# Kernel optimization log

Hardware: AMD Instinct MI355X
Metric: run time of the kernel (lower is better)

The kernel has to match this reference:

```python
import jax, jax.numpy as jnp
import numpy as np

N_NODES = 100000
N_EDGES = 1600000
C_IN, C_HID, C_OUT = 64, 64, 32


def _gcn_conv(x, src, dst, ew, W, b, n_nodes):
    """PyG GCNConv: add self-loops (weight 1), symmetric normalization,
    out[dst] += norm * (x @ W)[src], plus bias. Dropout omitted (eval mode)."""
    h = x @ W  # [N, C_out_layer]
    loop = jnp.arange(n_nodes, dtype=src.dtype)
    src_a = jnp.concatenate([src, loop])
    dst_a = jnp.concatenate([dst, loop])
    ew_a = jnp.concatenate([ew, jnp.ones((n_nodes,), dtype=ew.dtype)])
    # degree over incoming (dst) side, weighted
    deg = jax.ops.segment_sum(ew_a, dst_a, num_segments=n_nodes)
    dinv = jnp.where(deg > 0, jax.lax.rsqrt(deg), 0.0)
    norm = dinv[src_a] * ew_a * dinv[dst_a]  # [E+N]
    msg = h[src_a] * norm[:, None]           # gather + scale: [E+N, C]
    out = jax.ops.segment_sum(msg, dst_a, num_segments=n_nodes)  # scatter-add
    return out + b


def setup_inputs() -> dict:
    key = jax.random.key(0)
    k1, k2, k3, k4, k5, k6, k7 = jax.random.split(key, 7)
    x = jax.random.normal(k1, (N_NODES, C_IN), dtype=jnp.float32)
    edge_index = jax.random.randint(k2, (2, N_EDGES), 0, N_NODES, dtype=jnp.int64)
    edge_attr = jax.random.uniform(k3, (N_EDGES,), dtype=jnp.float32)
    s1 = 1.0 / np.sqrt(C_IN)
    s2 = 1.0 / np.sqrt(C_HID)
    W1 = jax.random.uniform(k4, (C_IN, C_HID), jnp.float32, -s1, s1)
    b1 = jnp.zeros((C_HID,), dtype=jnp.float32)
    W2 = jax.random.uniform(k5, (C_HID, C_OUT), jnp.float32, -s2, s2)
    b2 = jnp.zeros((C_OUT,), dtype=jnp.float32)
    return {"x": x, "edge_index": edge_index, "edge_attr": edge_attr,
            "W1": W1, "b1": b1, "W2": W2, "b2": b2}


def reference(x, edge_index, edge_attr, W1, b1, W2, b2):
    n = x.shape[0]
    src, dst = edge_index[0], edge_index[1]
    h = _gcn_conv(x, src, dst, edge_attr, W1, b1, n)
    h = jax.nn.relu(h)  # dropout is identity in eval mode
    out = _gcn_conv(h, src, dst, edge_attr, W2, b2, n)
    return out
```

## Files before the change

kernel.cpp:

```cpp
#include <hip/hip_runtime.h>
#include <hip/hip_fp16.h>


#define TPB 256
#define TPB_P 512
#define TPB_S 1024
#define BSH2 9
#define BN2 512
#define NBC 256
#define PCHUNK 4096
#define CAP2 9728

typedef union { uint2 u; __half2 h[2]; } hpack;
typedef union { uint4 u; __half2 h[4]; } hpack8;
typedef union { int4 q; int2 p[2]; } epack;

__global__ __launch_bounds__(256) void k_binit(int* __restrict__ bpos) {
  int i = threadIdx.x;
  if (i < NBC) bpos[i] = i * CAP2;
}

__global__ __launch_bounds__(TPB_P) void k_part(const int* __restrict__ si,
                                                const int* __restrict__ di,
                                                const float* __restrict__ ew,
                                                int* __restrict__ bpos,
                                                int2* __restrict__ tin, int e) {
  __shared__ int hcnt[NBC];
  __shared__ int lst0[NBC];
  __shared__ int lcur[NBC];
  __shared__ int hbase[NBC];
  __shared__ int2 se[PCHUNK];
  __shared__ unsigned char sbk[PCHUNK];
  int t = threadIdx.x;
  int lo = blockIdx.x * PCHUNK;
  int hi = lo + PCHUNK; if (hi > e) hi = e;
  int cn = hi - lo;
  if (t < NBC) hcnt[t] = 0;
  __syncthreads();
  for (int i = lo + t; i < hi; i += TPB_P) atomicAdd(&hcnt[di[i] >> BSH2], 1);
  __syncthreads();
  int c = (t < NBC) ? hcnt[t] : 0;
  for (int off = 1; off < NBC; off <<= 1) {
    int u = (t >= off && t < NBC) ? hcnt[t - off] : 0;
    __syncthreads();
    if (t < NBC) hcnt[t] += u;
    __syncthreads();
  }
  if (t < NBC) {
    int ex = hcnt[t] - c;
    lst0[t] = ex;
    lcur[t] = 0;
    hbase[t] = c ? atomicAdd(&bpos[t], c) : 0;
  }
  __syncthreads();
  for (int i = lo + t; i < hi; i += TPB_P) {
    int d = di[i];
    int bk = d >> BSH2;
    int loc = atomicAdd(&lcur[bk], 1);
    int p = lst0[bk] + loc;
    se[p] = make_int2(si[i] | ((d & (BN2 - 1)) << 17), __float_as_int(ew[i]));
    sbk[p] = (unsigned char)bk;
  }
  __syncthreads();
  for (int p = t; p < cn; p += TPB_P) {
    int bk = sbk[p];
    tin[hbase[bk] + (p - lst0[bk])] = se[p];
  }
}

__global__ __launch_bounds__(TPB_S) void k_sortb(const int2* __restrict__ tin,
                                                 const int* __restrict__ bpos,
                                                 int2* __restrict__ colpk,
                                                 int2* __restrict__ rowseg,
                                                 float* __restrict__ dinv, int n) {
  __shared__ int cnt[BN2];
  __shared__ float degw[BN2];
  __shared__ int cur[BN2];
  __shared__ int ls[BN2];
  int b = blockIdx.x, t = threadIdx.x;
  if (t < BN2) { cnt[t] = 0; degw[t] = 1.0f; }
  __syncthreads();
  int jb = b * CAP2, je = bpos[b];
  for (int j = jb + t; j < je; j += TPB_S) {
    int2 p = tin[j];
    int dl = p.x >> 17;
    atomicAdd(&cnt[dl], 1);
    atomicAdd(&degw[dl], __int_as_float(p.y));
  }
  __syncthreads();
  int c = (t < BN2) ? cnt[t] : 0;
  int c2 = (c + 1) & ~1;
  if (t < BN2) ls[t] = c2;
  __syncthreads();
  for (int off = 1; off < BN2; off <<= 1) {
    int u = (t >= off && t < BN2) ? ls[t - off] : 0;
    __syncthreads();
    if (t < BN2) ls[t] += u;
    __syncthreads();
  }
  int base = b << BSH2;
  if (t < BN2) {
    int start = jb + ls[t] - c2;
    cur[t] = start;
    int node = base + t;
    if (node < n) {
      rowseg[node] = make_int2(start, start + c2);
      dinv[node] = rsqrtf(degw[t]);
    }
    if (c & 1) colpk[start + c] = make_int2(0, 0);
  }
  __syncthreads();
  for (int j = jb + t; j < je; j += TPB_S) {
    int2 p = tin[j];
    int dl = p.x >> 17;
    int pos = atomicAdd(&cur[dl], 1);
    colpk[pos] = make_int2(p.x & 0x1FFFF, p.y);
  }
}

__global__ __launch_bounds__(TPB) void k_gemm1(const float* __restrict__ x,
                                               const float* __restrict__ W1,
                                               const float* __restrict__ dinv,
                                               __half* __restrict__ g1h, int n) {
  __shared__ float Wl[64 * 64];
  int t = threadIdx.x;
  {
    const float4* W4 = (const float4*)W1;
    float4* Wl4 = (float4*)Wl;
#pragma unroll
    for (int i = 0; i < 4; ++i) Wl4[t + TPB * i] = W4[t + TPB * i];
  }
  __syncthreads();
  int r = blockIdx.x * 16 + (t >> 4);
  if (r >= n) return;
  int c0 = (t & 15) << 2;
  const float4* xr = (const float4*)(x + (size_t)r * 64);
  float ax = 0.f, ay = 0.f, az = 0.f, aw = 0.f;
#pragma unroll
  for (int kk = 0; kk < 16; ++kk) {
    float4 xv = xr[kk];
    const float* w = &Wl[(kk * 4) * 64 + c0];
    float4 w0 = *(const float4*)(w);
    float4 w1 = *(const float4*)(w + 64);
    float4 w2 = *(const float4*)(w + 128);
    float4 w3 = *(const float4*)(w + 192);
    ax += xv.x * w0.x + xv.y * w1.x + xv.z * w2.x + xv.w * w3.x;
    ay += xv.x * w0.y + xv.y * w1.y + xv.z * w2.y + xv.w * w3.y;
    az += xv.x * w0.z + xv.y * w1.z + xv.z * w2.z + xv.w * w3.z;
    aw += xv.x * w0.w + xv.y * w1.w + xv.z * w2.w + xv.w * w3.w;
  }
  float dv = dinv[r];
  hpack pk;
  pk.h[0] = __floats2half2_rn(dv * ax, dv * ay);
  pk.h[1] = __floats2half2_rn(dv * az, dv * aw);
  *(uint2*)(g1h + (size_t)r * 64 + c0) = pk.u;
}

__global__ __launch_bounds__(TPB) void k_gather64(const __half* __restrict__ g1h,
                                                  const int2* __restrict__ colpk,
                                                  const int2* __restrict__ rowseg,
                                                  float* __restrict__ acc, int n) {
  int t = threadIdx.x;
  int r = blockIdx.x * 32 + (t >> 3);
  if (r >= n) return;
  int c0 = (t & 7) << 3;
  float a[8];
  {
    hpack8 s; s.u = *(const uint4*)(g1h + (size_t)r * 64 + c0);
#pragma unroll
    for (int k = 0; k < 4; ++k) {
      float2 f = __half22float2(s.h[k]);
      a[2 * k] = f.x; a[2 * k + 1] = f.y;
    }
  }
  int2 seg = rowseg[r];
  int j = seg.x;
  for (; j + 7 < seg.y; j += 8) {
    epack q0; q0.q = *(const int4*)(colpk + j);
    epack q1; q1.q = *(const int4*)(colpk + j + 2);
    epack q2; q2.q = *(const int4*)(colpk + j + 4);
    epack q3; q3.q = *(const int4*)(colpk + j + 6);
    hpack8 u0; u0.u = *(const uint4*)(g1h + (size_t)q0.p[0].x * 64 + c0);
    hpack8 u1; u1.u = *(const uint4*)(g1h + (size_t)q0.p[1].x * 64 + c0);
    hpack8 u2; u2.u = *(const uint4*)(g1h + (size_t)q1.p[0].x * 64 + c0);
    hpack8 u3; u3.u = *(const uint4*)(g1h + (size_t)q1.p[1].x * 64 + c0);
    hpack8 u4; u4.u = *(const uint4*)(g1h + (size_t)q2.p[0].x * 64 + c0);
    hpack8 u5; u5.u = *(const uint4*)(g1h + (size_t)q2.p[1].x * 64 + c0);
    hpack8 u6; u6.u = *(const uint4*)(g1h + (size_t)q3.p[0].x * 64 + c0);
    hpack8 u7; u7.u = *(const uint4*)(g1h + (size_t)q3.p[1].x * 64 + c0);
    float w0 = __int_as_float(q0.p[0].y), w1 = __int_as_float(q0.p[1].y);
    float w2 = __int_as_float(q1.p[0].y), w3 = __int_as_float(q1.p[1].y);
    float w4 = __int_as_float(q2.p[0].y), w5 = __int_as_float(q2.p[1].y);
    float w6 = __int_as_float(q3.p[0].y), w7 = __int_as_float(q3.p[1].y);
#pragma unroll
    for (int k = 0; k < 4; ++k) {
      float2 f;
      f = __half22float2(u0.h[k]); a[2*k] += w0 * f.x; a[2*k+1] += w0 * f.y;
      f = __half22float2(u1.h[k]); a[2*k] += w1 * f.x; a[2*k+1] += w1 * f.y;
      f = __half22float2(u2.h[k]); a[2*k] += w2 * f.x; a[2*k+1] += w2 * f.y;
      f = __half22float2(u3.h[k]); a[2*k] += w3 * f.x; a[2*k+1] += w3 * f.y;
      f = __half22float2(u4.h[k]); a[2*k] += w4 * f.x; a[2*k+1] += w4 * f.y;
      f = __half22float2(u5.h[k]); a[2*k] += w5 * f.x; a[2*k+1] += w5 * f.y;
      f = __half22float2(u6.h[k]); a[2*k] += w6 * f.x; a[2*k+1] += w6 * f.y;
      f = __half22float2(u7.h[k]); a[2*k] += w7 * f.x; a[2*k+1] += w7 * f.y;
    }
  }
  for (; j + 1 < seg.y; j += 2) {
    epack q0; q0.q = *(const int4*)(colpk + j);
    float w0 = __int_as_float(q0.p[0].y), w1 = __int_as_float(q0.p[1].y);
    hpack8 u0; u0.u = *(const uint4*)(g1h + (size_t)q0.p[0].x * 64 + c0);
    hpack8 u1; u1.u = *(const uint4*)(g1h + (size_t)q0.p[1].x * 64 + c0);
#pragma unroll
    for (int k = 0; k < 4; ++k) {
      float2 f;
      f = __half22float2(u0.h[k]); a[2*k] += w0 * f.x; a[2*k+1] += w0 * f.y;
      f = __half22float2(u1.h[k]); a[2*k] += w1 * f.x; a[2*k+1] += w1 * f.y;
    }
  }
  float* op = acc + (size_t)r * 64 + c0;
  *(float4*)(op)     = make_float4(a[0], a[1], a[2], a[3]);
  *(float4*)(op + 4) = make_float4(a[4], a[5], a[6], a[7]);
}

__global__ __launch_bounds__(TPB) void k_gemm2(const float* __restrict__ acc1,
                                               const float* __restrict__ W2,
                                               const float* __restrict__ b1,
                                               const float* __restrict__ dinv,
                                               __half* __restrict__ g2h, int n) {
  __shared__ float Wl[64 * 32];
  __shared__ float b1l[64];
  int t = threadIdx.x;
  {
    const float4* W4 = (const float4*)W2;
    float4* Wl4 = (float4*)Wl;
#pragma unroll
    for (int i = 0; i < 2; ++i) Wl4[t + TPB * i] = W4[t + TPB * i];
    if (t < 64) b1l[t] = b1[t];
  }
  __syncthreads();
  int r = blockIdx.x * 32 + (t >> 3);
  if (r >= n) return;
  int c0 = (t & 7) << 2;
  float dv = dinv[r];
  const float4* ar = (const float4*)(acc1 + (size_t)r * 64);
  float ax = 0.f, ay = 0.f, az = 0.f, aw = 0.f;
#pragma unroll
  for (int kk = 0; kk < 16; ++kk) {
    float4 v = ar[kk];
    float x0 = fmaxf(dv * v.x + b1l[4 * kk + 0], 0.f);
    float x1 = fmaxf(dv * v.y + b1l[4 * kk + 1], 0.f);
    float x2 = fmaxf(dv * v.z + b1l[4 * kk + 2], 0.f);
    float x3 = fmaxf(dv * v.w + b1l[4 * kk + 3], 0.f);
    const float* w = &Wl[(kk * 4) * 32 + c0];
    float4 w0 = *(const float4*)(w);
    float4 w1 = *(const float4*)(w + 32);
    float4 w2 = *(const float4*)(w + 64);
    float4 w3 = *(const float4*)(w + 96);
    ax += x0 * w0.x + x1 * w1.x + x2 * w2.x + x3 * w3.x;
    ay += x0 * w0.y + x1 * w1.y + x2 * w2.y + x3 * w3.y;
    az += x0 * w0.z + x1 * w1.z + x2 * w2.z + x3 * w3.z;
    aw += x0 * w0.w + x1 * w1.w + x2 * w2.w + x3 * w3.w;
  }
  hpack pk;
  pk.h[0] = __floats2half2_rn(dv * ax, dv * ay);
  pk.h[1] = __floats2half2_rn(dv * az, dv * aw);
  *(uint2*)(g2h + (size_t)r * 32 + c0) = pk.u;
}

__global__ __launch_bounds__(TPB) void k_gather32(const __half* __restrict__ g2h,
                                                  const int2* __restrict__ colpk,
                                                  const int2* __restrict__ rowseg,
                                                  const float* __restrict__ dinv,
                                                  const float* __restrict__ b2,
                                                  float* __restrict__ out, int n) {
  int t = threadIdx.x;
  int r = blockIdx.x * 64 + (t >> 2);
  if (r >= n) return;
  int c0 = (t & 3) << 3;
  float a[8];
  {
    hpack8 s; s.u = *(const uint4*)(g2h + (size_t)r * 32 + c0);
#pragma unroll
    for (int k = 0; k < 4; ++k) {
      float2 f = __half22float2(s.h[k]);
      a[2 * k] = f.x; a[2 * k + 1] = f.y;
    }
  }
  int2 seg = rowseg[r];
  int j = seg.x;
  for (; j + 7 < seg.y; j += 8) {
    epack q0; q0.q = *(const int4*)(colpk + j);
    epack q1; q1.q = *(const int4*)(colpk + j + 2);
    epack q2; q2.q = *(const int4*)(colpk + j + 4);
    epack q3; q3.q = *(const int4*)(colpk + j + 6);
    hpack8 u0; u0.u = *(const uint4*)(g2h + (size_t)q0.p[0].x * 32 + c0);
    hpack8 u1; u1.u = *(const uint4*)(g2h + (size_t)q0.p[1].x * 32 + c0);
    hpack8 u2; u2.u = *(const uint4*)(g2h + (size_t)q1.p[0].x * 32 + c0);
    hpack8 u3; u3.u = *(const uint4*)(g2h + (size_t)q1.p[1].x * 32 + c0);
    hpack8 u4; u4.u = *(const uint4*)(g2h + (size_t)q2.p[0].x * 32 + c0);
    hpack8 u5; u5.u = *(const uint4*)(g2h + (size_t)q2.p[1].x * 32 + c0);
    hpack8 u6; u6.u = *(const uint4*)(g2h + (size_t)q3.p[0].x * 32 + c0);
    hpack8 u7; u7.u = *(const uint4*)(g2h + (size_t)q3.p[1].x * 32 + c0);
    float w0 = __int_as_float(q0.p[0].y), w1 = __int_as_float(q0.p[1].y);
    float w2 = __int_as_float(q1.p[0].y), w3 = __int_as_float(q1.p[1].y);
    float w4 = __int_as_float(q2.p[0].y), w5 = __int_as_float(q2.p[1].y);
    float w6 = __int_as_float(q3.p[0].y), w7 = __int_as_float(q3.p[1].y);
#pragma unroll
    for (int k = 0; k < 4; ++k) {
      float2 f;
      f = __half22float2(u0.h[k]); a[2*k] += w0 * f.x; a[2*k+1] += w0 * f.y;
      f = __half22float2(u1.h[k]); a[2*k] += w1 * f.x; a[2*k+1] += w1 * f.y;
      f = __half22float2(u2.h[k]); a[2*k] += w2 * f.x; a[2*k+1] += w2 * f.y;
      f = __half22float2(u3.h[k]); a[2*k] += w3 * f.x; a[2*k+1] += w3 * f.y;
      f = __half22float2(u4.h[k]); a[2*k] += w4 * f.x; a[2*k+1] += w4 * f.y;
      f = __half22float2(u5.h[k]); a[2*k] += w5 * f.x; a[2*k+1] += w5 * f.y;
      f = __half22float2(u6.h[k]); a[2*k] += w6 * f.x; a[2*k+1] += w6 * f.y;
      f = __half22float2(u7.h[k]); a[2*k] += w7 * f.x; a[2*k+1] += w7 * f.y;
    }
  }
  for (; j + 1 < seg.y; j += 2) {
    epack q0; q0.q = *(const int4*)(colpk + j);
    float w0 = __int_as_float(q0.p[0].y), w1 = __int_as_float(q0.p[1].y);
    hpack8 u0; u0.u = *(const uint4*)(g2h + (size_t)q0.p[0].x * 32 + c0);
    hpack8 u1; u1.u = *(const uint4*)(g2h + (size_t)q0.p[1].x * 32 + c0);
#pragma unroll
    for (int k = 0; k < 4; ++k) {
      float2 f;
      f = __half22float2(u0.h[k]); a[2*k] += w0 * f.x; a[2*k+1] += w0 * f.y;
      f = __half22float2(u1.h[k]); a[2*k] += w1 * f.x; a[2*k+1] += w1 * f.y;
    }
  }
  float dv = dinv[r];
  const float4* b24 = (const float4*)(b2 + c0);
  float4 bb0 = b24[0], bb1 = b24[1];
  float* op = out + (size_t)r * 32 + c0;
  *(float4*)(op)     = make_float4(dv * a[0] + bb0.x, dv * a[1] + bb0.y,
                                   dv * a[2] + bb0.z, dv * a[3] + bb0.w);
  *(float4*)(op + 4) = make_float4(dv * a[4] + bb1.x, dv * a[5] + bb1.y,
                                   dv * a[6] + bb1.z, dv * a[7] + bb1.w);
}

extern "C" void kernel_launch(void* const* d_in, const int* in_sizes, int n_in,
                              void* d_out, int out_size, void* d_ws, size_t ws_size,
                              hipStream_t stream) {
  const float* x  = (const float*)d_in[0];
  const int* ei   = (const int*)d_in[1];
  const float* ew = (const float*)d_in[2];
  const float* W1 = (const float*)d_in[3];
  const float* b1 = (const float*)d_in[4];
  const float* W2 = (const float*)d_in[5];
  const float* b2 = (const float*)d_in[6];
  float* out = (float*)d_out;

  const int n = in_sizes[0] / 64;
  const int e = in_sizes[1] / 2;
  const int* si = ei;
  const int* di = ei + e;
  const int NBc = (n + BN2 - 1) >> BSH2;

  float* ws = (float*)d_ws;
  const size_t NP = 100352;
  float*  dinv   = ws;
  __half* g1h    = (__half*)(ws + NP);
  float*  acc1   = ws + NP + (size_t)n * 32;
  int2*   rowseg = (int2*)(acc1 + (size_t)n * 64);
  int*    bpos   = (int*)(rowseg + NP);
  int2*   colpk  = (int2*)(bpos + 1024);
  int2*   tin    = (int2*)acc1;
  __half* g2h    = g1h;

  int gb_part = (e + PCHUNK - 1) / PCHUNK;
  int gb_g1 = (n + 15) / 16;
  int gb_g64 = (n + 31) / 32;
  int gb_g2 = (n + 31) / 32;
  int gb_g32 = (n + 63) / 64;

  k_binit<<<1, 256, 0, stream>>>(bpos);
  k_part<<<gb_part, TPB_P, 0, stream>>>(si, di, ew, bpos, tin, e);
  k_sortb<<<NBc, TPB_S, 0, stream>>>(tin, bpos, colpk, rowseg, dinv, n);
  k_gemm1<<<gb_g1, TPB, 0, stream>>>(x, W1, dinv, g1h, n);
  k_gather64<<<gb_g64, TPB, 0, stream>>>(g1h, colpk, rowseg, acc1, n);
  k_gemm2<<<gb_g2, TPB, 0, stream>>>(acc1, W2, b1, dinv, g2h, n);
  k_gather32<<<gb_g32, TPB, 0, stream>>>(g2h, colpk, rowseg, dinv, b2, out, n);
}
```

Measured before the change: 223.1 us.

## Fuse layer-1 gather with layer-2 GEMM via shared-memory staging

```diff
diff --git a/kernel.cpp b/kernel.cpp
--- a/kernel.cpp
+++ b/kernel.cpp
@@ -10,15 +10,11 @@
 #define NBC 256
 #define PCHUNK 4096
 #define CAP2 9728
+#define XSTR 68
 
 typedef union { uint2 u; __half2 h[2]; } hpack;
 typedef union { uint4 u; __half2 h[4]; } hpack8;
 typedef union { int4 q; int2 p[2]; } epack;
-
-__global__ __launch_bounds__(256) void k_binit(int* __restrict__ bpos) {
-  int i = threadIdx.x;
-  if (i < NBC) bpos[i] = i * CAP2;
-}
 
 __global__ __launch_bounds__(TPB_P) void k_part(const int* __restrict__ si,
                                                 const int* __restrict__ di,
@@ -50,7 +46,7 @@
     int ex = hcnt[t] - c;
     lst0[t] = ex;
     lcur[t] = 0;
-    hbase[t] = c ? atomicAdd(&bpos[t], c) : 0;
+    hbase[t] = c ? (t * CAP2 + atomicAdd(&bpos[t], c)) : 0;
   }
   __syncthreads();
   for (int i = lo + t; i < hi; i += TPB_P) {
@@ -80,7 +76,7 @@
   int b = blockIdx.x, t = threadIdx.x;
   if (t < BN2) { cnt[t] = 0; degw[t] = 1.0f; }
   __syncthreads();
-  int jb = b * CAP2, je = bpos[b];
+  int jb = b * CAP2, je = jb + bpos[b];
   for (int j = jb + t; j < je; j += TPB_S) {
     int2 p = tin[j];
     int dl = p.x >> 17;
@@ -156,115 +152,114 @@
   *(uint2*)(g1h + (size_t)r * 64 + c0) = pk.u;
 }
 
-__global__ __launch_bounds__(TPB) void k_gather64(const __half* __restrict__ g1h,
-                                                  const int2* __restrict__ colpk,
-                                                  const int2* __restrict__ rowseg,
-                                                  float* __restrict__ acc, int n) {
+__global__ __launch_bounds__(TPB) void k_gfuse(const __half* __restrict__ g1h,
+                                               const int2* __restrict__ colpk,
+                                               const int2* __restrict__ rowseg,
+                                               const float* __restrict__ dinv,
+                                               const float* __restrict__ W2,
+                                               const float* __restrict__ b1,
+                                               __half* __restrict__ g2h, int n) {
+  __shared__ float W2l[64 * 32];
+  __shared__ float b1l[64];
+  __shared__ float x2l[32 * XSTR];
   int t = threadIdx.x;
-  int r = blockIdx.x * 32 + (t >> 3);
-  if (r >= n) return;
+  {
+    const float4* W4 = (const float4*)W2;
+    float4* Wl4 = (float4*)W2l;
+#pragma unroll
+    for (int i = 0; i < 2; ++i) Wl4[t + TPB * i] = W4[t + TPB * i];
+    if (t < 64) b1l[t] = b1[t];
+  }
+  int node = t >> 3;
+  int r = blockIdx.x * 32 + node;
   int c0 = (t & 7) << 3;
+  bool valid = (r < n);
   float a[8];
-  {
+  float dv = 0.f;
+  if (valid) {
+    dv = dinv[r];
     hpack8 s; s.u = *(const uint4*)(g1h + (size_t)r * 64 + c0);
 #pragma unroll
     for (int k = 0; k < 4; ++k) {
       float2 f = __half22float2(s.h[k]);
       a[2 * k] = f.x; a[2 * k + 1] = f.y;
     }
-  }
-  int2 seg = rowseg[r];
-  int j = seg.x;
-  for (; j + 7 < seg.y; j += 8) {
-    epack q0; q0.q = *(const int4*)(colpk + j);
-    epack q1; q1.q = *(const int4*)(colpk + j + 2);
-    epack q2; q2.q = *(const int4*)(colpk + j + 4);
-    epack q3; q3.q = *(const int4*)(colpk + j + 6);
-    hpack8 u0; u0.u = *(const uint4*)(g1h + (size_t)q0.p[0].x * 64 + c0);
-    hpack8 u1; u1.u = *(const uint4*)(g1h + (size_t)q0.p[1].x * 64 + c0);
-    hpack8 u2; u2.u = *(const uint4*)(g1h + (size_t)q1.p[0].x * 64 + c0);
-    hpack8 u3; u3.u = *(const uint4*)(g1h + (size_t)q1.p[1].x * 64 + c0);
-    hpack8 u4; u4.u = *(const uint4*)(g1h + (size_t)q2.p[0].x * 64 + c0);
-    hpack8 u5; u5.u = *(const uint4*)(g1h + (size_t)q2.p[1].x * 64 + c0);
-    hpack8 u6; u6.u = *(const uint4*)(g1h + (size_t)q3.p[0].x * 64 + c0);
-    hpack8 u7; u7.u = *(const uint4*)(g1h + (size_t)q3.p[1].x * 64 + c0);
-    float w0 = __int_as_float(q0.p[0].y), w1 = __int_as_float(q0.p[1].y);
-    float w2 = __int_as_float(q1.p[0].y), w3 = __int_as_float(q1.p[1].y);
-    float w4 = __int_as_float(q2.p[0].y), w5 = __int_as_float(q2.p[1].y);
-    float w6 = __int_as_float(q3.p[0].y), w7 = __int_as_float(q3.p[1].y);
-#pragma unroll
-    for (int k = 0; k < 4; ++k) {
-      float2 f;
-      f = __half22float2(u0.h[k]); a[2*k] += w0 * f.x; a[2*k+1] += w0 * f.y;
-      f = __half22float2(u1.h[k]); a[2*k] += w1 * f.x; a[2*k+1] += w1 * f.y;
-      f = __half22float2(u2.h[k]); a[2*k] += w2 * f.x; a[2*k+1] += w2 * f.y;
-      f = __half22float2(u3.h[k]); a[2*k] += w3 * f.x; a[2*k+1] += w3 * f.y;
-      f = __half22float2(u4.h[k]); a[2*k] += w4 * f.x; a[2*k+1] += w4 * f.y;
-      f = __half22float2(u5.h[k]); a[2*k] += w5 * f.x; a[2*k+1] += w5 * f.y;
-      f = __half22float2(u6.h[k]); a[2*k] += w6 * f.x; a[2*k+1] += w6 * f.y;
-      f = __half22float2(u7.h[k]); a[2*k] += w7 * f.x; a[2*k+1] += w7 * f.y;
-    }
-  }
-  for (; j + 1 < seg.y; j += 2) {
-    epack q0; q0.q = *(const int4*)(colpk + j);
-    float w0 = __int_as_float(q0.p[0].y), w1 = __int_as_float(q0.p[1].y);
-    hpack8 u0; u0.u = *(const uint4*)(g1h + (size_t)q0.p[0].x * 64 + c0);
-    hpack8 u1; u1.u = *(const uint4*)(g1h + (size_t)q0.p[1].x * 64 + c0);
-#pragma unroll
-    for (int k = 0; k < 4; ++k) {
-      float2 f;
-      f = __half22float2(u0.h[k]); a[2*k] += w0 * f.x; a[2*k+1] += w0 * f.y;
-      f = __half22float2(u1.h[k]); a[2*k] += w1 * f.x; a[2*k+1] += w1 * f.y;
-    }
-  }
-  float* op = acc + (size_t)r * 64 + c0;
-  *(float4*)(op)     = make_float4(a[0], a[1], a[2], a[3]);
-  *(float4*)(op + 4) = make_float4(a[4], a[5], a[6], a[7]);
-}
-
-__global__ __launch_bounds__(TPB) void k_gemm2(const float* __restrict__ acc1,
-                                               const float* __restrict__ W2,
-                                               const float* __restrict__ b1,
-                                               const float* __restrict__ dinv,
-                                               __half* __restrict__ g2h, int n) {
-  __shared__ float Wl[64 * 32];
-  __shared__ float b1l[64];
-  int t = threadIdx.x;
-  {
-    const float4* W4 = (const float4*)W2;
-    float4* Wl4 = (float4*)Wl;
-#pragma unroll
-    for (int i = 0; i < 2; ++i) Wl4[t + TPB * i] = W4[t + TPB * i];
-    if (t < 64) b1l[t] = b1[t];
-  }
-  __syncthreads();
-  int r = blockIdx.x * 32 + (t >> 3);
-  if (r >= n) return;
-  int c0 = (t & 7) << 2;
-  float dv = dinv[r];
-  const float4* ar = (const float4*)(acc1 + (size_t)r * 64);
+    int2 seg = rowseg[r];
+    int j = seg.x;
+    for (; j + 7 < seg.y; j += 8) {
+      epack q0; q0.q = *(const int4*)(colpk + j);
+      epack q1; q1.q = *(const int4*)(colpk + j + 2);
+      epack q2; q2.q = *(const int4*)(colpk + j + 4);
+      epack q3; q3.q = *(const int4*)(colpk + j + 6);
+      hpack8 u0; u0.u = *(const uint4*)(g1h + (size_t)q0.p[0].x * 64 + c0);
+      hpack8 u1; u1.u = *(const uint4*)(g1h + (size_t)q0.p[1].x * 64 + c0);
+      hpack8 u2; u2.u = *(const uint4*)(g1h + (size_t)q1.p[0].x * 64 + c0);
+      hpack8 u3; u3.u = *(const uint4*)(g1h + (size_t)q1.p[1].x * 64 + c0);
+      hpack8 u4; u4.u = *(const uint4*)(g1h + (size_t)q2.p[0].x * 64 + c0);
+      hpack8 u5; u5.u = *(const uint4*)(g1h + (size_t)q2.p[1].x * 64 + c0);
+      hpack8 u6; u6.u = *(const uint4*)(g1h + (size_t)q3.p[0].x * 64 + c0);
+      hpack8 u7; u7.u = *(const uint4*)(g1h + (size_t)q3.p[1].x * 64 + c0);
+      float w0 = __int_as_float(q0.p[0].y), w1 = __int_as_float(q0.p[1].y);
+      float w2 = __int_as_float(q1.p[0].y), w3 = __int_as_float(q1.p[1].y);
+      float w4 = __int_as_float(q2.p[0].y), w5 = __int_as_float(q2.p[1].y);
+      float w6 = __int_as_float(q3.p[0].y), w7 = __int_as_float(q3.p[1].y);
+#pragma unroll
+      for (int k = 0; k < 4; ++k) {
+        float2 f;
+        f = __half22float2(u0.h[k]); a[2*k] += w0 * f.x; a[2*k+1] += w0 * f.y;
+        f = __half22float2(u1.h[k]); a[2*k] += w1 * f.x; a[2*k+1] += w1 * f.y;
+        f = __half22float2(u2.h[k]); a[2*k] += w2 * f.x; a[2*k+1] += w2 * f.y;
+        f = __half22float2(u3.h[k]); a[2*k] += w3 * f.x; a[2*k+1] += w3 * f.y;
+        f = __half22float2(u4.h[k]); a[2*k] += w4 * f.x; a[2*k+1] += w4 * f.y;
+        f = __half22float2(u5.h[k]); a[2*k] += w5 * f.x; a[2*k+1] += w5 * f.y;
+        f = __half22float2(u6.h[k]); a[2*k] += w6 * f.x; a[2*k+1] += w6 * f.y;
+        f = __half22float2(u7.h[k]); a[2*k] += w7 * f.x; a[2*k+1] += w7 * f.y;
+      }
+    }
+    for (; j + 1 < seg.y; j += 2) {
+      epack q0; q0.q = *(const int4*)(colpk + j);
+      float w0 = __int_as_float(q0.p[0].y), w1 = __int_as_float(q0.p[1].y);
+      hpack8 u0; u0.u = *(const uint4*)(g1h + (size_t)q0.p[0].x * 64 + c0);
+      hpack8 u1; u1.u = *(const uint4*)(g1h + (size_t)q0.p[1].x * 64 + c0);
+#pragma unroll
+      for (int k = 0; k < 4; ++k) {
+        float2 f;
+        f = __half22float2(u0.h[k]); a[2*k] += w0 * f.x; a[2*k+1] += w0 * f.y;
+        f = __half22float2(u1.h[k]); a[2*k] += w1 * f.x; a[2*k+1] += w1 * f.y;
+      }
+    }
+    float* xp = x2l + node * XSTR + c0;
+#pragma unroll
+    for (int k = 0; k < 8; k += 4) {
+      float4 v = {fmaxf(dv * a[k + 0] + b1l[c0 + k + 0], 0.f),
+                  fmaxf(dv * a[k + 1] + b1l[c0 + k + 1], 0.f),
+                  fmaxf(dv * a[k + 2] + b1l[c0 + k + 2], 0.f),
+                  fmaxf(dv * a[k + 3] + b1l[c0 + k + 3], 0.f)};
+      *(float4*)(xp + k) = v;
+    }
+  }
+  __syncthreads();
+  if (!valid) return;
+  int oc = (t & 7) << 2;
+  const float* xr = x2l + node * XSTR;
   float ax = 0.f, ay = 0.f, az = 0.f, aw = 0.f;
 #pragma unroll
   for (int kk = 0; kk < 16; ++kk) {
-    float4 v = ar[kk];
-    float x0 = fmaxf(dv * v.x + b1l[4 * kk + 0], 0.f);
-    float x1 = fmaxf(dv * v.y + b1l[4 * kk + 1], 0.f);
-    float x2 = fmaxf(dv * v.z + b1l[4 * kk + 2], 0.f);
-    float x3 = fmaxf(dv * v.w + b1l[4 * kk + 3], 0.f);
-    const float* w = &Wl[(kk * 4) * 32 + c0];
+    float4 xv = *(const float4*)(xr + 4 * kk);
+    const float* w = &W2l[(kk * 4) * 32 + oc];
     float4 w0 = *(const float4*)(w);
     float4 w1 = *(const float4*)(w + 32);
     float4 w2 = *(const float4*)(w + 64);
     float4 w3 = *(const float4*)(w + 96);
-    ax += x0 * w0.x + x1 * w1.x + x2 * w2.x + x3 * w3.x;
-    ay += x0 * w0.y + x1 * w1.y + x2 * w2.y + x3 * w3.y;
-    az += x0 * w0.z + x1 * w1.z + x2 * w2.z + x3 * w3.z;
-    aw += x0 * w0.w + x1 * w1.w + x2 * w2.w + x3 * w3.w;
+    ax += xv.x * w0.x + xv.y * w1.x + xv.z * w2.x + xv.w * w3.x;
+    ay += xv.x * w0.y + xv.y * w1.y + xv.z * w2.y + xv.w * w3.y;
+    az += xv.x * w0.z + xv.y * w1.z + xv.z * w2.z + xv.w * w3.z;
+    aw += xv.x * w0.w + xv.y * w1.w + xv.z * w2.w + xv.w * w3.w;
   }
   hpack pk;
   pk.h[0] = __floats2half2_rn(dv * ax, dv * ay);
   pk.h[1] = __floats2half2_rn(dv * az, dv * aw);
-  *(uint2*)(g2h + (size_t)r * 32 + c0) = pk.u;
+  *(uint2*)(g2h + (size_t)r * 32 + oc) = pk.u;
 }
 
 __global__ __launch_bounds__(TPB) void k_gather32(const __half* __restrict__ g2h,
@@ -362,24 +357,22 @@
   const size_t NP = 100352;
   float*  dinv   = ws;
   __half* g1h    = (__half*)(ws + NP);
-  float*  acc1   = ws + NP + (size_t)n * 32;
-  int2*   rowseg = (int2*)(acc1 + (size_t)n * 64);
+  int2*   rowseg = (int2*)(ws + NP + (size_t)n * 32);
   int*    bpos   = (int*)(rowseg + NP);
   int2*   colpk  = (int2*)(bpos + 1024);
-  int2*   tin    = (int2*)acc1;
+  int2*   tin    = colpk + (size_t)NBC * CAP2;
   __half* g2h    = g1h;
+  g2h = (__half*)(tin + (size_t)NBC * CAP2);
 
   int gb_part = (e + PCHUNK - 1) / PCHUNK;
   int gb_g1 = (n + 15) / 16;
-  int gb_g64 = (n + 31) / 32;
-  int gb_g2 = (n + 31) / 32;
+  int gb_gf = (n + 31) / 32;
   int gb_g32 = (n + 63) / 64;
 
-  k_binit<<<1, 256, 0, stream>>>(bpos);
+  hipMemsetAsync(bpos, 0, NBC * sizeof(int), stream);
   k_part<<<gb_part, TPB_P, 0, stream>>>(si, di, ew, bpos, tin, e);
   k_sortb<<<NBc, TPB_S, 0, stream>>>(tin, bpos, colpk, rowseg, dinv, n);
   k_gemm1<<<gb_g1, TPB, 0, stream>>>(x, W1, dinv, g1h, n);
-  k_gather64<<<gb_g64, TPB, 0, stream>>>(g1h, colpk, rowseg, acc1, n);
-  k_gemm2<<<gb_g2, TPB, 0, stream>>>(acc1, W2, b1, dinv, g2h, n);
+  k_gfuse<<<gb_gf, TPB, 0, stream>>>(g1h, colpk, rowseg, dinv, W2, b1, g2h, n);
   k_gather32<<<gb_g32, TPB, 0, stream>>>(g2h, colpk, rowseg, dinv, b2, out, n);
 }
```

Result: faster. 216.4 us (-3.0%).
